# Kernel optimization log

Measured on AMD Instinct MI355X. Metric: run time of the kernel, lower is better.

Reference implementation:

```python
import jax, jax.numpy as jnp
import numpy as np
from jax import lax

B, T, C, U = 32, 512, 4233, 64


def setup_inputs() -> dict:
    key = jax.random.key(0)
    k1, k2 = jax.random.split(key)
    logits = jax.random.normal(k1, (B, T, C), dtype=jnp.float32)
    ctc_logit = jax.nn.log_softmax(logits, axis=-1)  # [B, T, C] log-probs
    # labels in [1, C) so none equal blank (code treats blank-valued labels as pad)
    label = jax.random.randint(k2, (U, B), 1, C, dtype=jnp.int32)  # [U, B]
    return {"ctc_logit": ctc_logit, "label": label, "blank_id": 0}


def ctc_fa(ctc_logit, label, blank_id):
    pad_value = jnp.finfo(ctc_logit.dtype).min
    lab = label.T  # [B, U]
    lab = jnp.where(lab == blank_id, -1, lab)
    Bb, Uu = lab.shape
    Tt = ctc_logit.shape[1]
    Cc = ctc_logit.shape[2]
    yl = (lab >= 0).sum(1) * 2 + 1  # [B] extended label length
    # interleave blanks: [blank, l0, blank, l1, ..., blank] -> lab_T = 2U+1
    blanks = jnp.full_like(lab, blank_id)
    ext = jnp.stack([blanks, lab], axis=2).reshape(Bb, 2 * Uu)
    ext = jnp.pad(ext, ((0, 0), (0, 1)), constant_values=blank_id)  # [B, labT]
    labT = 2 * Uu + 1
    shifted2 = jnp.pad(ext, ((0, 0), (2, 0)), constant_values=-1)[:, :labT]
    cond = (ext == blank_id) | (ext == shifted2)  # [B, labT]
    ext_idx = ext % Cc  # mimic torch negative-index wrap for -1 pad labels
    # emission log-probs gathered per extended-label position: [B, T, labT]
    emit = jnp.take_along_axis(ctc_logit, ext_idx[:, None, :], axis=2)
    dp0 = jnp.full((Bb, labT), pad_value, ctc_logit.dtype)
    dp0 = dp0.at[:, 0].set(emit[:, 0, 0]).at[:, 1].set(emit[:, 0, 1])
    jrange = jnp.arange(labT)

    def shift(x, n):
        return jnp.pad(x, ((0, 0), (n, 0)), constant_values=pad_value)[:, :labT]

    def step(dp_prev, emit_t):
        s1 = shift(dp_prev, 1)
        s2 = shift(dp_prev, 2)
        a2 = jnp.stack([dp_prev, s1], axis=-1)          # [B, labT, 2]
        a3 = jnp.stack([dp_prev, s1, s2], axis=-1)      # [B, labT, 3]
        idx1 = jnp.argmax(a2, axis=-1)
        idx2 = jnp.argmax(a3, axis=-1)
        lse2 = jax.scipy.special.logsumexp(a2, axis=-1)
        lse3 = jax.scipy.special.logsumexp(a3, axis=-1)
        dp_t = emit_t + jnp.where(cond, lse2, lse3)
        bp_t = jrange[None, :] - jnp.where(cond, idx1, idx2)
        return dp_t, (dp_t, bp_t)

    emit_tbj = jnp.swapaxes(emit, 0, 1)  # [T, B, labT]
    dp_last, (_, bps) = lax.scan(step, dp0, emit_tbj[1:])
    bp0 = jnp.broadcast_to(jrange[None, None, :], (1, Bb, labT)).astype(bps.dtype)
    bp_all = jnp.concatenate([bp0, bps], axis=0)  # [T, B, labT]
    bi = jnp.arange(Bb)
    d1 = dp_last[bi, yl - 1]
    d2 = dp_last[bi, yl - 2]
    ctc_loss = -jnp.logaddexp(d1, d2)
    ctc_loss = 2 * ctc_loss / (yl - 1)
    # Viterbi backtrack -> hard alignment [B, T, labT]
    wi0 = jnp.where(d1 > d2, yl - 1, yl - 2)

    def bstep(wi, bp_t):
        align_t = (jrange[None, :] == wi[:, None]).astype(jnp.int32)
        wi_next = jnp.take_along_axis(bp_t, wi[:, None], axis=1)[:, 0]
        return wi_next, align_t

    _, align_ts = lax.scan(bstep, wi0, bp_all, reverse=True)  # [T, B, labT]
    align = jnp.swapaxes(align_ts, 0, 1)  # [B, T, labT]
    return align, ctc_loss


def reference(ctc_logit, label, blank_id):
    return ctc_fa(ctc_logit, label, blank_id)
```

## Files before the change

### kernel.cpp

```cpp
#include <hip/hip_runtime.h>
#include <math.h>

#define NB 32
#define NT 512
#define NC 4233
#define NU 64
#define LABT 129
#define PADV (-3.4028234663852886e38f)
#define SCANBLK 192

__global__ void ctc_prep_kernel(const int* __restrict__ label,
                                const int* __restrict__ blank_ptr,
                                int* __restrict__ ext_idx,
                                int* __restrict__ cond,
                                int* __restrict__ yl)
{
    const int b = blockIdx.x;
    const int j = threadIdx.x;
    const int blank = blank_ptr[0];

    if (j < 64) {
        int raw = label[j * NB + b];
        unsigned long long m = __ballot(raw != blank);
        if (j == 0) yl[b] = 2 * (int)__popcll(m) + 1;
    }

    if (j < LABT) {
        int extv;
        if ((j & 1) == 0) {
            extv = blank;
        } else {
            int raw = label[((j - 1) >> 1) * NB + b];
            extv = (raw == blank) ? -1 : raw;
        }
        int sh2;
        if (j < 2) {
            sh2 = -1;
        } else if (((j - 2) & 1) == 0) {
            sh2 = blank;
        } else {
            int raw2 = label[((j - 3) >> 1) * NB + b];
            sh2 = (raw2 == blank) ? -1 : raw2;
        }
        int c = (extv == blank) || (extv == sh2);
        int idx = extv % NC;
        if (idx < 0) idx += NC;
        ext_idx[b * LABT + j] = idx;
        cond[b * LABT + j]    = c;
    }
}

__global__ __launch_bounds__(SCANBLK)
void ctc_scan_kernel(const float* __restrict__ logit,
                     const int*   __restrict__ ext_idx,
                     const int*   __restrict__ cond,
                     const int*   __restrict__ yl,
                     int*   __restrict__ wout,
                     float* __restrict__ loss_out)
{
    __shared__ float dbuf[2][SCANBLK + 8];
    __shared__ unsigned long long bpm[NT][3][2];
    __shared__ int wl[NT];

    const int b = blockIdx.x;
    const int j = threadIdx.x;
    const bool act = (j < LABT);

    const int col = act ? ext_idx[b * LABT + j] : 0;
    const int cnd = act ? cond[b * LABT + j] : 1;

    const float* lb = logit + (size_t)b * NT * NC;

    float* pa = dbuf[0];
    float* pb = dbuf[1];

    float e0 = lb[col];
    pa[j] = (j <= 1) ? e0 : PADV;

    float r0 = lb[(size_t)1 * NC + col];
    float r1 = lb[(size_t)2 * NC + col];
    float r2 = lb[(size_t)3 * NC + col];
    float r3 = lb[(size_t)4 * NC + col];
    __syncthreads();

#define STEP(tcur, rr, tload)                                                  \
    do {                                                                       \
        float a  = pa[j];                                                      \
        float b1 = (j >= 1) ? pa[j - 1] : PADV;                                \
        float c2 = (j >= 2) ? pa[j - 2] : PADV;                                \
        float c2e = cnd ? PADV : c2;      \
        float m  = fmaxf(fmaxf(a, b1), c2e);                                   \
        float lse = m + logf(expf(a - m) + expf(b1 - m) + expf(c2e - m));      \
        int delta = (a >= b1 && a >= c2e) ? 0 : ((b1 >= c2e) ? 1 : 2);         \
        pb[j] = rr + lse;                                                      \
        unsigned long long mm0 = __ballot(delta & 1);                          \
        unsigned long long mm1 = __ballot(delta >> 1);                         \
        if ((j & 63) == 0) {                                                   \
            bpm[tcur][j >> 6][0] = mm0;                                        \
            bpm[tcur][j >> 6][1] = mm1;                                        \
        }                                                                      \
        if ((tload) < NT) rr = lb[(size_t)(tload) * NC + col];                 \
        __syncthreads();                                                       \
        float* tpp = pa; pa = pb; pb = tpp;                                    \
    } while (0)

    int t = 1;
    for (; t + 3 < NT; t += 4) {
        STEP(t,     r0, t + 4);
        STEP(t + 1, r1, t + 5);
        STEP(t + 2, r2, t + 6);
        STEP(t + 3, r3, t + 7);
    }
    STEP(t,     r0, NT);
    STEP(t + 1, r1, NT);
    STEP(t + 2, r2, NT);
#undef STEP

    if (j == 0) {
        int Y = yl[b];
        float d1 = pa[Y - 1];
        float d2 = pa[Y - 2];
        float mm = fmaxf(d1, d2);
        float la = mm + logf(expf(d1 - mm) + expf(d2 - mm));
        loss_out[b] = -la * 2.0f / (float)(Y - 1);

        int w = (d1 > d2) ? (Y - 1) : (Y - 2);
        for (int tt = NT - 1; tt >= 1; --tt) {
            wl[tt] = w;
            int wv = w >> 6, ln = w & 63;
            unsigned long long m0 = bpm[tt][wv][0];
            unsigned long long m1 = bpm[tt][wv][1];
            int dd = (int)((m0 >> ln) & 1ULL) + 2 * (int)((m1 >> ln) & 1ULL);
            w -= dd;
        }
        wl[0] = w;
    }
    __syncthreads();
    for (int tt = j; tt < NT; tt += SCANBLK) wout[b * NT + tt] = wl[tt];
}

__global__ void ctc_align_kernel(const int* __restrict__ w,
                                 float* __restrict__ out)
{
    int tid = blockIdx.x * blockDim.x + threadIdx.x;
    if (tid >= NB * NT * LABT) return;
    int j  = tid % LABT;
    int bt = tid / LABT;
    out[tid] = (j == w[bt]) ? 1.0f : 0.0f;
}

extern "C" void kernel_launch(void* const* d_in, const int* in_sizes, int n_in,
                              void* d_out, int out_size, void* d_ws, size_t ws_size,
                              hipStream_t stream)
{
    const float* logit = (const float*)d_in[0];
    const int*   label = (const int*)d_in[1];
    const int*   blank = (const int*)d_in[2];

    float* out = (float*)d_out;
    int*   ws  = (int*)d_ws;

    int* ext_idx = ws;
    int* cond    = ws + NB * LABT;
    int* yl      = ws + 2 * NB * LABT;
    int* w       = ws + 2 * NB * LABT + NB;

    ctc_prep_kernel<<<NB, SCANBLK, 0, stream>>>(label, blank, ext_idx, cond, yl);
    ctc_scan_kernel<<<NB, SCANBLK, 0, stream>>>(logit, ext_idx, cond, yl, w,
                                                out + NB * NT * LABT);
    int total = NB * NT * LABT;
    ctc_align_kernel<<<(total + 255) / 256, 256, 0, stream>>>(w, out);
}
```

Baseline: 490.7 us.

## Pre-gather emissions in parallel kernel, fuse alignment output, pipeline backtrack loads

A new wide kernel gathers the per-label emission log-probs into a compact [B,T,LABT] workspace. The serial 32-block scan then reads contiguous, likely L2-resident data instead of scattered logits from the large tensor. The backtrack now loads the bit-packed back-pointer rows from LDS four rows ahead as 128-bit loads, to hide LDS latency in the serial loop. The separate alignment kernel is removed and its one-hot output is written from the scan kernel. That saves a launch, but the 8 MB output is now written by only 32 blocks and needs an integer divide per element.

```diff
diff --git a/kernel.cpp b/kernel.cpp
--- a/kernel.cpp
+++ b/kernel.cpp
@@ -8,6 +8,7 @@
 #define LABT 129
 #define PADV (-3.4028234663852886e38f)
 #define SCANBLK 192
+#define EMIT_N (NB * NT * LABT)
 
 __global__ void ctc_prep_kernel(const int* __restrict__ label,
                                 const int* __restrict__ blank_ptr,
@@ -50,37 +51,49 @@
     }
 }
 
+__global__ __launch_bounds__(256)
+void ctc_gather_kernel(const float* __restrict__ logit,
+                       const int*   __restrict__ ext_idx,
+                       float*       __restrict__ emit)
+{
+    int tid = blockIdx.x * 256 + threadIdx.x;
+    if (tid >= EMIT_N) return;
+    int bt = tid / LABT;
+    int j  = tid - bt * LABT;
+    int b  = bt / NT;
+    int col = ext_idx[b * LABT + j];
+    emit[tid] = logit[(size_t)bt * NC + col];
+}
+
 __global__ __launch_bounds__(SCANBLK)
-void ctc_scan_kernel(const float* __restrict__ logit,
-                     const int*   __restrict__ ext_idx,
+void ctc_scan_kernel(const float* __restrict__ emit,
                      const int*   __restrict__ cond,
                      const int*   __restrict__ yl,
-                     int*   __restrict__ wout,
+                     float* __restrict__ out,
                      float* __restrict__ loss_out)
 {
     __shared__ float dbuf[2][SCANBLK + 8];
-    __shared__ unsigned long long bpm[NT][3][2];
+    __shared__ __align__(16) unsigned long long bpm[NT][3][2];
     __shared__ int wl[NT];
 
     const int b = blockIdx.x;
     const int j = threadIdx.x;
     const bool act = (j < LABT);
-
-    const int col = act ? ext_idx[b * LABT + j] : 0;
+    const int jc = act ? j : 0;
     const int cnd = act ? cond[b * LABT + j] : 1;
 
-    const float* lb = logit + (size_t)b * NT * NC;
+    const float* eb = emit + (size_t)b * (NT * LABT);
 
     float* pa = dbuf[0];
     float* pb = dbuf[1];
 
-    float e0 = lb[col];
+    float e0 = eb[jc];
     pa[j] = (j <= 1) ? e0 : PADV;
 
-    float r0 = lb[(size_t)1 * NC + col];
-    float r1 = lb[(size_t)2 * NC + col];
-    float r2 = lb[(size_t)3 * NC + col];
-    float r3 = lb[(size_t)4 * NC + col];
+    float r0 = eb[1 * LABT + jc];
+    float r1 = eb[2 * LABT + jc];
+    float r2 = eb[3 * LABT + jc];
+    float r3 = eb[4 * LABT + jc];
     __syncthreads();
 
 #define STEP(tcur, rr, tload)                                                  \
@@ -99,7 +112,7 @@
             bpm[tcur][j >> 6][0] = mm0;                                        \
             bpm[tcur][j >> 6][1] = mm1;                                        \
         }                                                                      \
-        if ((tload) < NT) rr = lb[(size_t)(tload) * NC + col];                 \
+        if ((tload) < NT) rr = eb[(tload) * LABT + jc];                        \
         __syncthreads();                                                       \
         float* tpp = pa; pa = pb; pb = tpp;                                    \
     } while (0)
@@ -125,28 +138,51 @@
         loss_out[b] = -la * 2.0f / (float)(Y - 1);
 
         int w = (d1 > d2) ? (Y - 1) : (Y - 2);
-        for (int tt = NT - 1; tt >= 1; --tt) {
-            wl[tt] = w;
-            int wv = w >> 6, ln = w & 63;
-            unsigned long long m0 = bpm[tt][wv][0];
-            unsigned long long m1 = bpm[tt][wv][1];
-            int dd = (int)((m0 >> ln) & 1ULL) + 2 * (int)((m1 >> ln) & 1ULL);
-            w -= dd;
+        const ulonglong2* bp2 = (const ulonglong2*)&bpm[0][0][0];
+
+#define BLOAD(s0, s1, s2, row) do {                                            \
+        const ulonglong2* rp_ = bp2 + 3 * (row);                               \
+        s0 = rp_[0]; s1 = rp_[1]; s2 = rp_[2];                                 \
+    } while (0)
+#define BPROC(qa, qb, qc, row) do {                                            \
+        wl[row] = w;                                                           \
+        int wv_ = w >> 6, ln_ = w & 63;                                        \
+        unsigned long long m0_ = (wv_ == 0) ? qa.x : (wv_ == 1) ? qb.x : qc.x; \
+        unsigned long long m1_ = (wv_ == 0) ? qa.y : (wv_ == 1) ? qb.y : qc.y; \
+        w -= (int)((m0_ >> ln_) & 1ULL) + 2 * (int)((m1_ >> ln_) & 1ULL);      \
+    } while (0)
+
+        ulonglong2 q00, q01, q02, q10, q11, q12, q20, q21, q22, q30, q31, q32;
+        BLOAD(q00, q01, q02, NT - 1);
+        BLOAD(q10, q11, q12, NT - 2);
+        BLOAD(q20, q21, q22, NT - 3);
+        BLOAD(q30, q31, q32, NT - 4);
+        int tt;
+        for (tt = NT - 1; tt >= 8; tt -= 4) {
+            BPROC(q00, q01, q02, tt    ); BLOAD(q00, q01, q02, tt - 4);
+            BPROC(q10, q11, q12, tt - 1); BLOAD(q10, q11, q12, tt - 5);
+            BPROC(q20, q21, q22, tt - 2); BLOAD(q20, q21, q22, tt - 6);
+            BPROC(q30, q31, q32, tt - 3); BLOAD(q30, q31, q32, tt - 7);
         }
+        BPROC(q00, q01, q02, 7); BLOAD(q00, q01, q02, 3);
+        BPROC(q10, q11, q12, 6); BLOAD(q10, q11, q12, 2);
+        BPROC(q20, q21, q22, 5); BLOAD(q20, q21, q22, 1);
+        BPROC(q30, q31, q32, 4);
+        BPROC(q00, q01, q02, 3);
+        BPROC(q10, q11, q12, 2);
+        BPROC(q20, q21, q22, 1);
         wl[0] = w;
+#undef BLOAD
+#undef BPROC
     }
     __syncthreads();
-    for (int tt = j; tt < NT; tt += SCANBLK) wout[b * NT + tt] = wl[tt];
-}
-
-__global__ void ctc_align_kernel(const int* __restrict__ w,
-                                 float* __restrict__ out)
-{
-    int tid = blockIdx.x * blockDim.x + threadIdx.x;
-    if (tid >= NB * NT * LABT) return;
-    int j  = tid % LABT;
-    int bt = tid / LABT;
-    out[tid] = (j == w[bt]) ? 1.0f : 0.0f;
+
+    float* outA = out + (size_t)b * (NT * LABT);
+    for (int p = j; p < NT * LABT; p += SCANBLK) {
+        int tr = p / LABT;
+        int jj = p - tr * LABT;
+        outA[p] = (jj == wl[tr]) ? 1.0f : 0.0f;
+    }
 }
 
 extern "C" void kernel_launch(void* const* d_in, const int* in_sizes, int n_in,
@@ -158,16 +194,13 @@
     const int*   blank = (const int*)d_in[2];
 
     float* out = (float*)d_out;
-    int*   ws  = (int*)d_ws;
-
-    int* ext_idx = ws;
-    int* cond    = ws + NB * LABT;
-    int* yl      = ws + 2 * NB * LABT;
-    int* w       = ws + 2 * NB * LABT + NB;
+
+    float* emit    = (float*)d_ws;
+    int*   ext_idx = (int*)(emit + EMIT_N);
+    int*   cond    = ext_idx + NB * LABT;
+    int*   yl      = cond + NB * LABT;
 
     ctc_prep_kernel<<<NB, SCANBLK, 0, stream>>>(label, blank, ext_idx, cond, yl);
-    ctc_scan_kernel<<<NB, SCANBLK, 0, stream>>>(logit, ext_idx, cond, yl, w,
-                                                out + NB * NT * LABT);
-    int total = NB * NT * LABT;
-    ctc_align_kernel<<<(total + 255) / 256, 256, 0, stream>>>(w, out);
-}
+    ctc_gather_kernel<<<EMIT_N / 256, 256, 0, stream>>>(logit, ext_idx, emit);
+    ctc_scan_kernel<<<NB, SCANBLK, 0, stream>>>(emit, cond, yl, out, out + EMIT_N);
+}
```

Result: slower. 542.7 us (+10.6%).

## Pre-gather emissions and run CTC scan in a single wavefront

Applied to the files above, without the earlier changes.

Adds a fully parallel gather kernel that pulls the per-label emission log-probs into a compact workspace. The Viterbi/forward scan then runs in one 64-lane wavefront per batch, with each lane holding two lattice positions in registers and exchanging neighbours via shuffles instead of shared memory plus __syncthreads. The backtrack is software-pipelined with prefetched bitmask rows. The alignment output is zero-filled and scattered inside the scan kernel, which drops the separate align kernel. The change removes per-step block barriers and strided logit loads from the serial critical path, at the cost of an extra global workspace round trip and only 32 single-wave blocks doing the output writes.

```diff
diff --git a/kernel.cpp b/kernel.cpp
--- a/kernel.cpp
+++ b/kernel.cpp
@@ -7,146 +7,173 @@
 #define NU 64
 #define LABT 129
 #define PADV (-3.4028234663852886e38f)
-#define SCANBLK 192
+#define EMIT_N (NB * NT * LABT)
 
-__global__ void ctc_prep_kernel(const int* __restrict__ label,
-                                const int* __restrict__ blank_ptr,
-                                int* __restrict__ ext_idx,
-                                int* __restrict__ cond,
-                                int* __restrict__ yl)
+__global__ __launch_bounds__(256)
+void ctc_gather_kernel(const float* __restrict__ logit,
+                       const int*   __restrict__ label,
+                       const int*   __restrict__ blank_ptr,
+                       float*       __restrict__ emitP,
+                       float*       __restrict__ emitL)
 {
+    int tid = blockIdx.x * 256 + threadIdx.x;
+    if (tid >= EMIT_N) return;
+    int bt = tid / LABT;
+    int j  = tid - bt * LABT;
+    int b  = bt / NT;
+    int blank = blank_ptr[0];
+    int col;
+    if (j & 1) {
+        int raw = label[((j - 1) >> 1) * NB + b];
+        int ev  = (raw == blank) ? -1 : raw;
+        col = ev % NC;
+        if (col < 0) col += NC;
+    } else {
+        col = blank;
+    }
+    float v = logit[(size_t)bt * NC + col];
+    if (j < 128) emitP[(size_t)bt * 128 + j] = v;
+    else         emitL[bt] = v;
+}
+
+__global__ __launch_bounds__(64)
+void ctc_scan_kernel(const float* __restrict__ emitP,
+                     const float* __restrict__ emitL,
+                     const int*   __restrict__ label,
+                     const int*   __restrict__ blank_ptr,
+                     float* __restrict__ out,
+                     float* __restrict__ loss_out)
+{
+    __shared__ __align__(16) unsigned long long bpm[NT][4];
+    __shared__ int   wl[NT];
+    __shared__ float fdp[132];
+
     const int b = blockIdx.x;
-    const int j = threadIdx.x;
+    const int l = threadIdx.x;
     const int blank = blank_ptr[0];
 
-    if (j < 64) {
-        int raw = label[j * NB + b];
-        unsigned long long m = __ballot(raw != blank);
-        if (j == 0) yl[b] = 2 * (int)__popcll(m) + 1;
-    }
+    int raw = label[l * NB + b];
+    unsigned long long nbmask = __ballot(raw != blank);
+    const int Y = 2 * (int)__popcll(nbmask) + 1;
+    int ev  = (raw == blank) ? -1 : raw;
+    int pev = __shfl_up(ev, 1);
+    if (l == 0) pev = -1;
+    const bool cndO = (ev == blank) || (ev == pev);
 
-    if (j < LABT) {
-        int extv;
-        if ((j & 1) == 0) {
-            extv = blank;
-        } else {
-            int raw = label[((j - 1) >> 1) * NB + b];
-            extv = (raw == blank) ? -1 : raw;
-        }
-        int sh2;
-        if (j < 2) {
-            sh2 = -1;
-        } else if (((j - 2) & 1) == 0) {
-            sh2 = blank;
-        } else {
-            int raw2 = label[((j - 3) >> 1) * NB + b];
-            sh2 = (raw2 == blank) ? -1 : raw2;
-        }
-        int c = (extv == blank) || (extv == sh2);
-        int idx = extv % NC;
-        if (idx < 0) idx += NC;
-        ext_idx[b * LABT + j] = idx;
-        cond[b * LABT + j]    = c;
-    }
-}
+    const float2* ep = (const float2*)(emitP + (size_t)b * NT * 128) + l;
+    const float*  el = emitL + (size_t)b * NT;
 
-__global__ __launch_bounds__(SCANBLK)
-void ctc_scan_kernel(const float* __restrict__ logit,
-                     const int*   __restrict__ ext_idx,
-                     const int*   __restrict__ cond,
-                     const int*   __restrict__ yl,
-                     int*   __restrict__ wout,
-                     float* __restrict__ loss_out)
-{
-    __shared__ float dbuf[2][SCANBLK + 8];
-    __shared__ unsigned long long bpm[NT][3][2];
-    __shared__ int wl[NT];
+    float2 e00 = ep[0];
+    float v0 = (l == 0) ? e00.x : PADV;
+    float v1 = (l == 0) ? e00.y : PADV;
+    float v2 = PADV;
 
-    const int b = blockIdx.x;
-    const int j = threadIdx.x;
-    const bool act = (j < LABT);
+    float2 r0 = ep[1 * 64], r1 = ep[2 * 64], r2 = ep[3 * 64], r3 = ep[4 * 64];
+    float  q0 = el[1], q1 = el[2], q2 = el[3], q3 = el[4];
 
-    const int col = act ? ext_idx[b * LABT + j] : 0;
-    const int cnd = act ? cond[b * LABT + j] : 1;
-
-    const float* lb = logit + (size_t)b * NT * NC;
-
-    float* pa = dbuf[0];
-    float* pb = dbuf[1];
-
-    float e0 = lb[col];
-    pa[j] = (j <= 1) ? e0 : PADV;
-
-    float r0 = lb[(size_t)1 * NC + col];
-    float r1 = lb[(size_t)2 * NC + col];
-    float r2 = lb[(size_t)3 * NC + col];
-    float r3 = lb[(size_t)4 * NC + col];
-    __syncthreads();
-
-#define STEP(tcur, rr, tload)                                                  \
+#define STEP(tcur, rr, qq, tload)                                              \
     do {                                                                       \
-        float a  = pa[j];                                                      \
-        float b1 = (j >= 1) ? pa[j - 1] : PADV;                                \
-        float c2 = (j >= 2) ? pa[j - 2] : PADV;                                \
-        float c2e = cnd ? PADV : c2;      \
-        float m  = fmaxf(fmaxf(a, b1), c2e);                                   \
-        float lse = m + logf(expf(a - m) + expf(b1 - m) + expf(c2e - m));      \
-        int delta = (a >= b1 && a >= c2e) ? 0 : ((b1 >= c2e) ? 1 : 2);         \
-        pb[j] = rr + lse;                                                      \
-        unsigned long long mm0 = __ballot(delta & 1);                          \
-        unsigned long long mm1 = __ballot(delta >> 1);                         \
-        if ((j & 63) == 0) {                                                   \
-            bpm[tcur][j >> 6][0] = mm0;                                        \
-            bpm[tcur][j >> 6][1] = mm1;                                        \
+        float u1 = __shfl_up(v1, 1);                                           \
+        u1 = (l == 0) ? PADV : u1;                               \
+                              \
+        float mE   = fmaxf(v0, u1);                                            \
+        float lseE = mE + logf(1.0f + expf(-fabsf(v0 - u1)));                  \
+        unsigned long long bE = __ballot(v0 < u1);                             \
+                       \
+        float c2e = cndO ? PADV : u1;                                          \
+        float mO  = fmaxf(fmaxf(v1, v0), c2e);                                 \
+        float lseO = mO + logf(expf(v1 - mO) + expf(v0 - mO) + expf(c2e - mO));\
+        unsigned long long gAB = __ballot(v1 >= v0);                           \
+        unsigned long long gAC = __ballot(v1 >= c2e);                          \
+        unsigned long long gBC = __ballot(v0 >= c2e);                          \
+                                    \
+        float mL   = fmaxf(v2, v1);                                            \
+        float lseL = mL + logf(1.0f + expf(-fabsf(v2 - v1)));                  \
+        unsigned long long bL = __ballot(v2 < v1);                             \
+        v0 = rr.x + lseE;                                                      \
+        v1 = rr.y + lseO;                                                      \
+        v2 = qq   + lseL;                                                      \
+        if (l == 0) {                                                          \
+            unsigned long long t0m = gAB & gAC;                                \
+            bpm[tcur][0] = bE;                                                 \
+            bpm[tcur][1] = ~t0m & gBC;                                         \
+            bpm[tcur][2] = ~t0m & ~gBC;                                        \
+            bpm[tcur][3] = (bL >> 63);                                         \
         }                                                                      \
-        if ((tload) < NT) rr = lb[(size_t)(tload) * NC + col];                 \
-        __syncthreads();                                                       \
-        float* tpp = pa; pa = pb; pb = tpp;                                    \
+        if ((tload) < NT) { rr = ep[(tload) * 64]; qq = el[(tload)]; }         \
     } while (0)
 
     int t = 1;
     for (; t + 3 < NT; t += 4) {
-        STEP(t,     r0, t + 4);
-        STEP(t + 1, r1, t + 5);
-        STEP(t + 2, r2, t + 6);
-        STEP(t + 3, r3, t + 7);
+        STEP(t,     r0, q0, t + 4);
+        STEP(t + 1, r1, q1, t + 5);
+        STEP(t + 2, r2, q2, t + 6);
+        STEP(t + 3, r3, q3, t + 7);
     }
-    STEP(t,     r0, NT);
-    STEP(t + 1, r1, NT);
-    STEP(t + 2, r2, NT);
+    STEP(t,     r0, q0, NT);
+    STEP(t + 1, r1, q1, NT);
+    STEP(t + 2, r2, q2, NT);
 #undef STEP
 
-    if (j == 0) {
-        int Y = yl[b];
-        float d1 = pa[Y - 1];
-        float d2 = pa[Y - 2];
+    fdp[2 * l]     = v0;
+    fdp[2 * l + 1] = v1;
+    if (l == 63) fdp[128] = v2;
+    __syncthreads();
+
+    float* outA = out + (size_t)b * (NT * LABT);
+    {
+        float4 z4; z4.x = 0.f; z4.y = 0.f; z4.z = 0.f; z4.w = 0.f;
+        float4* o4 = (float4*)outA;
+        for (int p = l; p < (NT * LABT) / 4; p += 64) o4[p] = z4;
+    }
+
+    if (l == 0) {
+        int i2 = Y - 2; if (i2 < 0) i2 += LABT;
+        float d1 = fdp[Y - 1];
+        float d2 = fdp[i2];
         float mm = fmaxf(d1, d2);
         float la = mm + logf(expf(d1 - mm) + expf(d2 - mm));
         loss_out[b] = -la * 2.0f / (float)(Y - 1);
 
-        int w = (d1 > d2) ? (Y - 1) : (Y - 2);
-        for (int tt = NT - 1; tt >= 1; --tt) {
-            wl[tt] = w;
-            int wv = w >> 6, ln = w & 63;
-            unsigned long long m0 = bpm[tt][wv][0];
-            unsigned long long m1 = bpm[tt][wv][1];
-            int dd = (int)((m0 >> ln) & 1ULL) + 2 * (int)((m1 >> ln) & 1ULL);
-            w -= dd;
+        int w = (d1 > d2) ? (Y - 1) : i2;
+        const ulonglong2* bp2 = (const ulonglong2*)&bpm[0][0];
+
+#define BLOAD(qa, qb, row) do { qa = bp2[2 * (row)]; qb = bp2[2 * (row) + 1]; } while (0)
+#define BPROC(qa, qb, row) do {                                                \
+        wl[row] = w;                                                           \
+        int lw_ = w >> 1;                                                      \
+        int dE_ = (w == 128) ? (int)qb.y : (int)((qa.x >> lw_) & 1ULL);        \
+        int dO_ = (int)((qa.y >> lw_) & 1ULL) + 2 * (int)((qb.x >> lw_) & 1ULL);\
+        w -= (w & 1) ? dO_ : dE_;                                              \
+    } while (0)
+
+        ulonglong2 a0, b0, a1, b1, a2, b2, a3, b3;
+        BLOAD(a0, b0, NT - 1);
+        BLOAD(a1, b1, NT - 2);
+        BLOAD(a2, b2, NT - 3);
+        BLOAD(a3, b3, NT - 4);
+        int tt;
+        for (tt = NT - 1; tt >= 8; tt -= 4) {
+            BPROC(a0, b0, tt    ); BLOAD(a0, b0, tt - 4);
+            BPROC(a1, b1, tt - 1); BLOAD(a1, b1, tt - 5);
+            BPROC(a2, b2, tt - 2); BLOAD(a2, b2, tt - 6);
+            BPROC(a3, b3, tt - 3); BLOAD(a3, b3, tt - 7);
         }
+        BPROC(a0, b0, 7); BLOAD(a0, b0, 3);
+        BPROC(a1, b1, 6); BLOAD(a1, b1, 2);
+        BPROC(a2, b2, 5); BLOAD(a2, b2, 1);
+        BPROC(a3, b3, 4);
+        BPROC(a0, b0, 3);
+        BPROC(a1, b1, 2);
+        BPROC(a2, b2, 1);
         wl[0] = w;
+#undef BLOAD
+#undef BPROC
     }
     __syncthreads();
-    for (int tt = j; tt < NT; tt += SCANBLK) wout[b * NT + tt] = wl[tt];
-}
 
-__global__ void ctc_align_kernel(const int* __restrict__ w,
-                                 float* __restrict__ out)
-{
-    int tid = blockIdx.x * blockDim.x + threadIdx.x;
-    if (tid >= NB * NT * LABT) return;
-    int j  = tid % LABT;
-    int bt = tid / LABT;
-    out[tid] = (j == w[bt]) ? 1.0f : 0.0f;
+    for (int t2 = l; t2 < NT; t2 += 64)
+        outA[(size_t)t2 * LABT + wl[t2]] = 1.0f;
 }
 
 extern "C" void kernel_launch(void* const* d_in, const int* in_sizes, int n_in,
@@ -158,16 +185,12 @@
     const int*   blank = (const int*)d_in[2];
 
     float* out = (float*)d_out;
-    int*   ws  = (int*)d_ws;
 
-    int* ext_idx = ws;
-    int* cond    = ws + NB * LABT;
-    int* yl      = ws + 2 * NB * LABT;
-    int* w       = ws + 2 * NB * LABT + NB;
+    float* emitP = (float*)d_ws;
+    float* emitL = emitP + (size_t)NB * NT * 128;
 
-    ctc_prep_kernel<<<NB, SCANBLK, 0, stream>>>(label, blank, ext_idx, cond, yl);
-    ctc_scan_kernel<<<NB, SCANBLK, 0, stream>>>(logit, ext_idx, cond, yl, w,
-                                                out + NB * NT * LABT);
-    int total = NB * NT * LABT;
-    ctc_align_kernel<<<(total + 255) / 256, 256, 0, stream>>>(w, out);
+    ctc_gather_kernel<<<(EMIT_N + 255) / 256, 256, 0, stream>>>(
+        logit, label, blank, emitP, emitL);
+    ctc_scan_kernel<<<NB, 64, 0, stream>>>(
+        emitP, emitL, label, blank, out, out + (size_t)NB * NT * LABT);
 }
```

Measured after the change: 566.9 us. 15.5% more time.
